# Optimization experiments

Measured on AMD Instinct MI355X. Metric: run time of the kernel, lower is better.

The kernel has to match this reference:

```python
import jax, jax.numpy as jnp
import numpy as np
import math

PERIODS = [4, 2, 1]          # period_num[-3:] sorted desc
SEQ, PRED, CH = 192, 96, 8
TOPM, DM = 20, 512
N_TRAIN, BSZ = 10000, 32


def decompose_mg(data):
    # data: [N, L, C] -> mg: [P, N, L, C], offset-removed (last step per period)
    N, L, C = data.shape
    mgs = []
    for g in PERIODS:
        cur = data.reshape(N, L // g, g, C).mean(axis=2)   # pooled
        cur = jnp.repeat(cur, g, axis=1)                   # repeat_interleave
        mgs.append(cur)
    mg = jnp.stack(mgs, axis=0)                            # [P, N, L, C]
    offset = mg[:, :, -1:, :]
    return mg - offset


def l2norm(x, eps=1e-12):
    n = jnp.sqrt(jnp.sum(x * x, axis=-1, keepdims=True))
    return x / jnp.maximum(n, eps)


def setup_inputs() -> dict:
    key = jax.random.key(0)
    ks = jax.random.split(key, 10)
    F = SEQ * CH
    return {
        "x": jax.random.normal(ks[0], (BSZ, SEQ, CH), dtype=jnp.float32),
        "index": jax.random.randint(ks[1], (BSZ,), 0, N_TRAIN),
        "train_data_all": jax.random.normal(ks[2], (N_TRAIN, SEQ, CH), dtype=jnp.float32),
        "y_data_all": jax.random.normal(ks[3], (N_TRAIN, PRED, CH), dtype=jnp.float32),
        "W_sim": jax.random.normal(ks[4], (F, F), dtype=jnp.float32) / math.sqrt(F),
        "b_sim": jax.random.normal(ks[5], (F,), dtype=jnp.float32) * 0.01,
        "Wq": jax.random.normal(ks[6], (CH, DM), dtype=jnp.float32) / math.sqrt(CH),
        "bq": jax.random.normal(ks[7], (DM,), dtype=jnp.float32) * 0.01,
        "Wk": jax.random.normal(ks[8], (CH, DM), dtype=jnp.float32) / math.sqrt(CH),
        "bk": jax.random.normal(ks[9], (DM,), dtype=jnp.float32) * 0.01,
    }


def reference(x, index, train_data_all, y_data_all, W_sim, b_sim, Wq, bq, Wk, bk):
    P = len(PERIODS)
    bsz = x.shape[0]
    n_train = train_data_all.shape[0]

    # multi-period decomposition (prepare_dataset + retrieve)
    train_mg = decompose_mg(train_data_all)   # [P, N, SEQ, CH]
    y_mg = decompose_mg(y_data_all)           # [P, N, PRED, CH]
    x_mg = decompose_mg(x)                    # [P, B, SEQ, CH]

    # periodic_batch_corr: shared linear then cosine similarity
    bx = x_mg.reshape(P, bsz, -1) @ W_sim + b_sim           # [P, B, F]
    ax = train_mg.reshape(P, n_train, -1) @ W_sim + b_sim   # [P, N, F]
    sim = jnp.einsum('pbf,pnf->pbn', l2norm(bx), l2norm(ax))

    # self-exclusion sliding mask (train=True)
    win = 2 * (SEQ + PRED) - 1
    slid = jnp.arange(win)[None, :] + (index - SEQ - PRED + 1)[:, None]
    slid = jnp.clip(slid, 0, n_train - 1)
    mask = jnp.zeros((bsz, n_train), dtype=bool).at[
        jnp.arange(bsz)[:, None], slid].set(True)
    sim = jnp.where(mask[None], -jnp.inf, sim)

    # top-m retrieval
    _, topm_idx = jax.lax.top_k(sim, TOPM)                  # [P, B, TOPM]

    # gather neighbors per period
    gather = jax.vmap(lambda src, i: src[i])                # over period axis
    k = gather(train_mg, topm_idx)                          # [P, B, M, SEQ, CH]
    v = gather(y_mg, topm_idx)                              # [P, B, M, PRED, CH]

    # cross attention (shared projections across periods)
    q_emb = x_mg @ Wq + bq                                  # [P, B, S, D]
    k_emb = k @ Wk + bk                                     # [P, B, M, T, D]
    scores = jnp.einsum('pbsd,pbmtd->pbsmt', q_emb, k_emb) / math.sqrt(DM)
    S = scores.shape[2]
    w = jax.nn.softmax(scores.reshape(P, bsz, S, TOPM * S), axis=-1)
    w = w.reshape(P, bsz, S, TOPM, S)
    nw = w.sum(axis=-1).sum(axis=2)                         # [P, B, M]
    nw = jax.nn.softmax(nw, axis=-1)
    out = jnp.einsum('pbm,pbmlc->pblc', nw, v)              # [P, B, PRED, CH]
    return out
```

## Files before the change

### kernel.cpp

```cpp
#include <hip/hip_runtime.h>
#include <hip/hip_bf16.h>
#include <math.h>

#define NPER 3
#define SEQL 192
#define PREDL 96
#define CH 8
#define FD 1536
#define NT 10000
#define BS 32
#define PB 96
#define TOPM 20
#define DM 512
#define HALFW 287
#define NROWS 30000
#define NRP2 10112
#define NRB2 79
#define NCB 12
#define PCOLS 24
#define NWG2 (NRB2*NCB)
#define NJ 3840
#define K0R 384
#define K1R 768
#define K2R 1536
#define KS 16
#define NCH 8
#define CHSZ (NT/NCH)
#define NWTG 4080
#define NB_DOT (3*NRB2)
#define BUFSZ (2*128*32)
#define RSQRT_DM 0.04419417382415922f

typedef __attribute__((ext_vector_type(8))) short bf16x8;
typedef __attribute__((ext_vector_type(4))) float f32x4;
typedef __attribute__((address_space(3))) short lds_short_t;
typedef __attribute__((address_space(1))) const short glb_short_t;

__device__ inline float bflo(unsigned u){ return __uint_as_float(u << 16); }
__device__ inline float bfhi(unsigned u){ return __uint_as_float(u & 0xFFFF0000u); }
__device__ inline float bf2f(unsigned short u){ return __uint_as_float((unsigned)u << 16); }
__device__ inline unsigned short f2bf(float v){
  __hip_bfloat16 h = __float2bfloat16(v);
  return *reinterpret_cast<unsigned short*>(&h);
}

template<int L>
__device__ __forceinline__ void dec_body(const float* __restrict__ data,
                                         float* __restrict__ mg,
                                         __hip_bfloat16* __restrict__ m0,
                                         __hip_bfloat16* __restrict__ m1,
                                         __hip_bfloat16* __restrict__ m2,
                                         __hip_bfloat16* __restrict__ trH,
                                         __hip_bfloat16* __restrict__ trL,
                                         int N, int n, float* fpool) {
  float* row = fpool;
  float* m4  = fpool + L*CH;
  float* m2s = fpool + L*CH + (L/4)*CH;
  const float* src = data + (size_t)n*L*CH;
  for (int e = threadIdx.x; e < L*CH/4; e += 256)
    *reinterpret_cast<float4*>(&row[e*4]) = *reinterpret_cast<const float4*>(&src[e*4]);
  __syncthreads();
  for (int i = threadIdx.x; i < (L/4)*CH; i += 256) {
    int j = i >> 3, c = i & 7;
    m4[i] = (row[(4*j)*CH+c] + row[(4*j+1)*CH+c] + row[(4*j+2)*CH+c] + row[(4*j+3)*CH+c]) * 0.25f;
  }
  for (int i = threadIdx.x; i < (L/2)*CH; i += 256) {
    int j = i >> 3, c = i & 7;
    m2s[i] = (row[(2*j)*CH+c] + row[(2*j+1)*CH+c]) * 0.5f;
  }
  __syncthreads();
  if (mg) {
    size_t plane = (size_t)N*L*CH;
    size_t base  = (size_t)n*L*CH;
    for (int e = threadIdx.x; e < L*CH/4; e += 256) {
      int i = e*4;
      int l = i >> 3, c0 = i & 7;
      float v0[4], v1[4], v2[4];
      #pragma unroll
      for (int j=0;j<4;j++) {
        int c = c0 + j;
        v0[j] = m4[(l>>2)*CH+c] - m4[(L/4-1)*CH+c];
        v1[j] = m2s[(l>>1)*CH+c] - m2s[(L/2-1)*CH+c];
        v2[j] = row[i+j] - row[(L-1)*CH+c];
      }
      *reinterpret_cast<float4*>(&mg[base+i])           = make_float4(v0[0],v0[1],v0[2],v0[3]);
      *reinterpret_cast<float4*>(&mg[plane+base+i])     = make_float4(v1[0],v1[1],v1[2],v1[3]);
      *reinterpret_cast<float4*>(&mg[2*plane+base+i])   = make_float4(v2[0],v2[1],v2[2],v2[3]);
    }
  }
  if (m0) {
    unsigned short* p0 = (unsigned short*)m0 + (size_t)n*K0R;
    unsigned short* p1 = (unsigned short*)m1 + (size_t)n*K1R;
    unsigned short* p2 = (unsigned short*)m2 + (size_t)n*K2R;
    for (int e = threadIdx.x; e < K0R/4; e += 256) {
      int i = e*4, c0 = i & 7;
      ushort4 u;
      u.x = f2bf(m4[i]   - m4[(L/4-1)*CH + c0]);
      u.y = f2bf(m4[i+1] - m4[(L/4-1)*CH + c0+1]);
      u.z = f2bf(m4[i+2] - m4[(L/4-1)*CH + c0+2]);
      u.w = f2bf(m4[i+3] - m4[(L/4-1)*CH + c0+3]);
      *reinterpret_cast<ushort4*>(&p0[i]) = u;
    }
    for (int e = threadIdx.x; e < K1R/4; e += 256) {
      int i = e*4, c0 = i & 7;
      ushort4 u;
      u.x = f2bf(m2s[i]   - m2s[(L/2-1)*CH + c0]);
      u.y = f2bf(m2s[i+1] - m2s[(L/2-1)*CH + c0+1]);
      u.z = f2bf(m2s[i+2] - m2s[(L/2-1)*CH + c0+2]);
      u.w = f2bf(m2s[i+3] - m2s[(L/2-1)*CH + c0+3]);
      *reinterpret_cast<ushort4*>(&p1[i]) = u;
    }
    for (int e = threadIdx.x; e < K2R/4; e += 256) {
      int i = e*4, c0 = i & 7;
      ushort4 u;
      u.x = f2bf(row[i]   - row[(L-1)*CH + c0]);
      u.y = f2bf(row[i+1] - row[(L-1)*CH + c0+1]);
      u.z = f2bf(row[i+2] - row[(L-1)*CH + c0+2]);
      u.w = f2bf(row[i+3] - row[(L-1)*CH + c0+3]);
      *reinterpret_cast<ushort4*>(&p2[i]) = u;
    }
  }
  if (trH) {
    unsigned short* h = (unsigned short*)trH + (size_t)n*L*CH;
    unsigned short* l = (unsigned short*)trL + (size_t)n*L*CH;
    for (int e = threadIdx.x; e < L*CH/4; e += 256) {
      int i = e*4;
      ushort4 uh, ul;
      uh.x = f2bf(row[i]);   ul.x = f2bf(row[i]   - bf2f(uh.x));
      uh.y = f2bf(row[i+1]); ul.y = f2bf(row[i+1] - bf2f(uh.y));
      uh.z = f2bf(row[i+2]); ul.z = f2bf(row[i+2] - bf2f(uh.z));
      uh.w = f2bf(row[i+3]); ul.w = f2bf(row[i+3] - bf2f(uh.w));
      *reinterpret_cast<ushort4*>(&h[i]) = uh;
      *reinterpret_cast<ushort4*>(&l[i]) = ul;
    }
  }
}

__device__ __forceinline__ void wtg_body(const float* __restrict__ W,
                                         __hip_bfloat16* __restrict__ wt0,
                                         __hip_bfloat16* __restrict__ wt1,
                                         __hip_bfloat16* __restrict__ wt2,
                                         const float* __restrict__ Wq,
                                         const float* __restrict__ bq,
                                         const float* __restrict__ Wk,
                                         const float* __restrict__ bk,
                                         float* __restrict__ cst,
                                         int wb, float* fpool) {
  int bxx = wb / 48, byy = wb % 48;
  if (bxx == 84) {
    if (byy != 0) return;
    int tt = threadIdx.x;
    if (tt < 64) {
      int c = tt >> 3, e = tt & 7;
      float s = 0.f;
      for (int d=0; d<DM; d++) s += Wq[c*DM+d] * Wk[e*DM+d];
      cst[tt] = s;
    } else if (tt < 72) {
      int c = tt - 64; float s=0.f;
      for (int d=0;d<DM;d++) s += Wq[c*DM+d]*bk[d];
      cst[tt] = s;
    } else if (tt < 80) {
      int e = tt - 72; float s=0.f;
      for (int d=0;d<DM;d++) s += Wk[e*DM+d]*bq[d];
      cst[tt] = s;
    } else if (tt == 80) {
      float s=0.f;
      for (int d=0;d<DM;d++) s += bq[d]*bk[d];
      cst[80] = s;
    }
    return;
  }
  int G, kr0, Kred;
  __hip_bfloat16* Wt;
  if (bxx < 12)      { G = 4; kr0 = bxx*32;      Kred = K0R; Wt = wt0; }
  else if (bxx < 36) { G = 2; kr0 = (bxx-12)*32; Kred = K1R; Wt = wt1; }
  else               { G = 1; kr0 = (bxx-36)*32; Kred = K2R; Wt = wt2; }
  int f0 = byy*32;
  int k0 = kr0*G;
  int tid = threadIdx.x, tx = tid & 31, ty = tid >> 5;
  for (int i = ty; i < 32*G; i += 8)
    fpool[i*33 + tx] = W[(size_t)(k0+i)*FD + f0 + tx];
  __syncthreads();
  for (int fl = ty; fl < 32; fl += 8) {
    float s = 0.f;
    for (int i=0;i<G;i++) s += fpool[(((tx>>3)*G+i)*8 + (tx&7))*33 + fl];
    Wt[(size_t)(f0+fl)*Kred + kr0 + tx] = __float2bfloat16(s);
  }
}

__global__ __launch_bounds__(256) void k_front(const float* __restrict__ x,
                                               const float* __restrict__ train,
                                               float* __restrict__ x_mg,
                                               __hip_bfloat16* __restrict__ m0,
                                               __hip_bfloat16* __restrict__ m1,
                                               __hip_bfloat16* __restrict__ m2,
                                               __hip_bfloat16* __restrict__ trH,
                                               __hip_bfloat16* __restrict__ trL,
                                               const float* __restrict__ W,
                                               __hip_bfloat16* __restrict__ wt0,
                                               __hip_bfloat16* __restrict__ wt1,
                                               __hip_bfloat16* __restrict__ wt2,
                                               const float* __restrict__ Wq,
                                               const float* __restrict__ bq,
                                               const float* __restrict__ Wk,
                                               const float* __restrict__ bk,
                                               float* __restrict__ cst) {
  __shared__ float fpool[128*33];
  int bid = blockIdx.x;
  if (bid < NT) {
    dec_body<SEQL>(train, nullptr, m0, m1, m2, trH, trL, NT, bid, fpool);
  } else if (bid < NT + NWTG) {
    wtg_body(W, wt0, wt1, wt2, Wq, bq, Wk, bk, cst, bid - NT, fpool);
  } else {
    dec_body<SEQL>(x, x_mg, nullptr, nullptr, nullptr, nullptr, nullptr,
                   BS, bid - NT - NWTG, fpool);
  }
}

__global__ __launch_bounds__(256) void k_bx_part(const float* __restrict__ xmg,
                                                 const float* __restrict__ W,
                                                 float* __restrict__ bxp) {
  __shared__ float xs[PB][17];
  __shared__ float Ws[16][65];
  int f0 = blockIdx.x * 64;
  int ks = blockIdx.y;
  int kbase = ks * (FD/KS);
  int tid = threadIdx.x;
  int fl = tid & 63, gp = tid >> 6;
  float acc[24];
  #pragma unroll
  for (int j=0;j<24;j++) acc[j]=0.f;
  for (int k0 = kbase; k0 < kbase + FD/KS; k0 += 16) {
    for (int e = tid; e < PB*16; e += 256) {
      int r = e >> 4, k = e & 15;
      xs[r][k] = xmg[(size_t)r*FD + k0 + k];
    }
    for (int e = tid; e < 16*64; e += 256) {
      int k = e >> 6, f = e & 63;
      Ws[k][f] = W[(size_t)(k0+k)*FD + f0 + f];
    }
    __syncthreads();
    #pragma unroll
    for (int kk = 0; kk < 16; kk++) {
      float w = Ws[kk][fl];
      #pragma unroll
      for (int j=0;j<24;j++) acc[j] += w * xs[gp + 4*j][kk];
    }
    __syncthreads();
  }
  #pragma unroll
  for (int j=0;j<24;j++) {
    int pb = gp + 4*j;
    bxp[((size_t)ks*PB + pb)*FD + f0 + fl] = acc[j];
  }
}

__global__ __launch_bounds__(256) void k_bxnorm(const float* __restrict__ bxp,
                                                const float* __restrict__ bsim,
                                                float* __restrict__ u_out,
                                                float* __restrict__ cpb) {
  __shared__ float rowv[FD];
  __shared__ float r1[256], r2[256];
  __shared__ float invs;
  int pb = blockIdx.x, tid = threadIdx.x;
  float s2 = 0.f, sb = 0.f;
  for (int f = tid; f < FD; f += 256) {
    float s = 0.f;
    #pragma unroll
    for (int ks=0; ks<KS; ks++) s += bxp[((size_t)ks*PB + pb)*FD + f];
    s += bsim[f];
    rowv[f] = s;
    s2 += s*s; sb += s*bsim[f];
  }
  r1[tid]=s2; r2[tid]=sb; __syncthreads();
  for (int off=128; off>0; off>>=1) {
    if (tid<off) { r1[tid]+=r1[tid+off]; r2[tid]+=r2[tid+off]; }
    __syncthreads();
  }
  if (tid==0) {
    float iv = 1.f / fmaxf(sqrtf(r1[0]), 1e-12f);
    invs = iv;
    cpb[pb] = r2[0] * iv;
  }
  __syncthreads();
  float iv = invs;
  for (int f = tid; f < FD; f += 256) u_out[(size_t)pb*FD + f] = rowv[f]*iv;
}

__global__ __launch_bounds__(256) void k_t_part(const float* __restrict__ u,
                                                const float* __restrict__ W,
                                                float* __restrict__ tp) {
  __shared__ float us[PB][17];
  __shared__ float Wt[64][17];
  int k0 = blockIdx.x * 64;
  int ks = blockIdx.y;
  int fbase = ks * (FD/KS);
  int tid = threadIdx.x;
  int kl = tid & 63, gp = tid >> 6;
  float acc[24];
  #pragma unroll
  for (int j=0;j<24;j++) acc[j]=0.f;
  for (int fc = fbase; fc < fbase + FD/KS; fc += 16) {
    for (int e = tid; e < PB*16; e += 256) {
      int r = e >> 4, f = e & 15;
      us[r][f] = u[(size_t)r*FD + fc + f];
    }
    for (int e = tid; e < 64*16; e += 256) {
      int k = e >> 4, f = e & 15;
      Wt[k][f] = W[(size_t)(k0+k)*FD + fc + f];
    }
    __syncthreads();
    #pragma unroll
    for (int ff = 0; ff < 16; ff++) {
      float w = Wt[kl][ff];
      #pragma unroll
      for (int j=0;j<24;j++) acc[j] += w * us[gp + 4*j][ff];
    }
    __syncthreads();
  }
  #pragma unroll
  for (int j=0;j<24;j++) {
    int pb = gp + 4*j;
    tp[((size_t)ks*PB + pb)*FD + k0 + kl] = acc[j];
  }
}

__global__ __launch_bounds__(192) void k_tred_adj(const float* __restrict__ tp,
                                                  __hip_bfloat16* __restrict__ tadjH,
                                                  __hip_bfloat16* __restrict__ tadjL) {
  __shared__ float ts[SEQL*CH];
  __shared__ float Tc[CH];
  int pb = blockIdx.x;
  int p = pb / BS;
  int g = (p==0) ? 4 : (p==1) ? 2 : 1;
  int l = threadIdx.x;
  #pragma unroll
  for (int c=0;c<CH;c++) {
    float s = 0.f;
    #pragma unroll
    for (int ks=0; ks<KS; ks++) s += tp[((size_t)ks*PB + pb)*FD + l*CH + c];
    ts[l*CH+c] = s;
  }
  __syncthreads();
  if (l < CH) {
    float s=0.f;
    for (int j=0;j<SEQL;j++) s += ts[j*CH+l];
    Tc[l] = s;
  }
  __syncthreads();
  int j0 = (l/g)*g;
  bool last = (j0 == SEQL-g);
  float ig = 1.f/(float)g;
  unsigned short* th = (unsigned short*)tadjH;
  unsigned short* tl = (unsigned short*)tadjL;
  #pragma unroll
  for (int c=0;c<CH;c++) {
    float s = 0.f;
    for (int jj=0;jj<g;jj++) s += ts[(j0+jj)*CH+c];
    float v = s*ig - (last ? Tc[c]*ig : 0.f);
    unsigned short hv = f2bf(v);
    th[(size_t)pb*FD + l*CH+c] = hv;
    tl[(size_t)pb*FD + l*CH+c] = f2bf(v - bf2f(hv));
  }
}

#define PIPE_SYNC_4()  do { asm volatile("s_waitcnt vmcnt(4)" ::: "memory"); \
                            __builtin_amdgcn_s_barrier(); \
                            __builtin_amdgcn_sched_barrier(0); } while(0)
#define PIPE_SYNC_0()  do { asm volatile("s_waitcnt vmcnt(0)" ::: "memory"); \
                            __builtin_amdgcn_s_barrier(); \
                            __builtin_amdgcn_sched_barrier(0); } while(0)

__device__ __forceinline__ void norm_body(const short* __restrict__ A,
                                          const short* __restrict__ B,
                                          int K, int p, int seg,
                                          const float* __restrict__ bsim,
                                          float* __restrict__ part,
                                          short* pool) {
  int q = NWG2 >> 3, r = NWG2 & 7;
  int xcd = seg & 7, pos = seg >> 3;
  int wgid = (xcd < r ? xcd*(q+1) : r*(q+1) + (xcd-r)*q) + pos;
  int rb = wgid / NCB, cb = wgid - rb*NCB;
  int row0 = rb*128, col0 = cb*128;
  int tid = threadIdx.x, lane = tid & 63, wid = tid >> 6;
  int wr = (wid>>1)*64, wc = (wid&1)*64;

  size_t aoff[2], boff[2];
  int ldsb[2];
  #pragma unroll
  for (int i=0;i<2;i++) {
    int lrow = (wid*2+i)*16 + (lane>>2);
    int sl = lane & 3;
    int ss = (sl - lrow - (lrow>>2)) & 3;
    aoff[i] = (size_t)(row0 + lrow)*K + 8*ss;
    boff[i] = (size_t)(col0 + lrow)*K + 8*ss;
    ldsb[i] = (wid*2+i)*16*32;
  }

  f32x4 acc[4][4];
  #pragma unroll
  for (int m=0;m<4;m++)
    #pragma unroll
    for (int n=0;n<4;n++) acc[m][n] = (f32x4){0.f,0.f,0.f,0.f};

  int kslot = lane >> 4;
  int nt = K >> 5;
  #pragma unroll
  for (int i=0;i<2;i++) {
    __builtin_amdgcn_global_load_lds((glb_short_t*)(A + aoff[i]),
                                     (lds_short_t*)&pool[ldsb[i]], 16, 0, 0);
    __builtin_amdgcn_global_load_lds((glb_short_t*)(B + boff[i]),
                                     (lds_short_t*)&pool[128*32 + ldsb[i]], 16, 0, 0);
  }
  #pragma unroll
  for (int i=0;i<2;i++) {
    __builtin_amdgcn_global_load_lds((glb_short_t*)(A + aoff[i] + 32),
                                     (lds_short_t*)&pool[BUFSZ + ldsb[i]], 16, 0, 0);
    __builtin_amdgcn_global_load_lds((glb_short_t*)(B + boff[i] + 32),
                                     (lds_short_t*)&pool[BUFSZ + 128*32 + ldsb[i]], 16, 0, 0);
  }
  PIPE_SYNC_4();
  int cur = 0;
  for (int t = 0; t < nt; ++t) {
    if (t + 2 < nt) {
      int nx = cur + 2; if (nx >= 3) nx -= 3;
      short* nb = pool + nx*BUFSZ;
      int kn = (t+2) << 5;
      #pragma unroll
      for (int i=0;i<2;i++) {
        __builtin_amdgcn_global_load_lds((glb_short_t*)(A + aoff[i] + kn),
                                         (lds_short_t*)&nb[ldsb[i]], 16, 0, 0);
        __builtin_amdgcn_global_load_lds((glb_short_t*)(B + boff[i] + kn),
                                         (lds_short_t*)&nb[128*32 + ldsb[i]], 16, 0, 0);
      }
    }
    const short* lA = pool + cur*BUFSZ;
    const short* lB = lA + 128*32;
    bf16x8 af[4], bfr[4];
    #pragma unroll
    for (int m=0;m<4;m++) {
      int rr = wr + m*16 + (lane&15);
      int s = (kslot + rr + (rr>>2)) & 3;
      af[m] = *(const bf16x8*)&lA[rr*32 + s*8];
    }
    #pragma unroll
    for (int n=0;n<4;n++) {
      int rr = wc + n*16 + (lane&15);
      int s = (kslot + rr + (rr>>2)) & 3;
      bfr[n] = *(const bf16x8*)&lB[rr*32 + s*8];
    }
    #pragma unroll
    for (int m=0;m<4;m++)
      #pragma unroll
      for (int n=0;n<4;n++)
        acc[m][n] = __builtin_amdgcn_mfma_f32_16x16x32_bf16(af[m], bfr[n], acc[m][n], 0, 0, 0);
    if (t + 1 < nt) {
      if (t + 2 < nt) PIPE_SYNC_4(); else PIPE_SYNC_0();
    }
    cur = (cur + 1 == 3) ? 0 : cur + 1;
  }

  float bv[4];
  #pragma unroll
  for (int n=0;n<4;n++) bv[n] = bsim[col0 + wc + n*16 + (lane&15)];
  int pslot = cb*2 + (wid&1);
  #pragma unroll
  for (int m=0;m<4;m++) {
    #pragma unroll
    for (int j=0;j<4;j++) {
      float s = 0.f;
      #pragma unroll
      for (int n=0;n<4;n++) { float v = acc[m][n][j] + bv[n]; s += v*v; }
      s += __shfl_xor(s, 1); s += __shfl_xor(s, 2);
      s += __shfl_xor(s, 4); s += __shfl_xor(s, 8);
      if ((lane & 15) == 0) {
        int rr = row0 + wr + m*16 + (lane>>4)*4 + j;
        part[((size_t)p*NRP2 + rr)*PCOLS + pslot] = s;
      }
    }
  }
}

__device__ __forceinline__ void dot_body(const short* __restrict__ A,
                                         const short* __restrict__ B,
                                         float* __restrict__ dst,
                                         int cbn, short* pool) {
  int col0 = cbn * 128;
  int tid = threadIdx.x, lane = tid & 63, wid = tid >> 6;
  int wr = (wid>>1)*64, wc = (wid&1)*64;

  size_t aoff[2], boff[2];
  int ldsb[2];
  #pragma unroll
  for (int i=0;i<2;i++) {
    int lrow = (wid*2+i)*16 + (lane>>2);
    int sl = lane & 3;
    int ss = (sl - lrow - (lrow>>2)) & 3;
    aoff[i] = (size_t)lrow*FD + 8*ss;
    boff[i] = (size_t)(col0 + lrow)*FD + 8*ss;
    ldsb[i] = (wid*2+i)*16*32;
  }

  f32x4 acc[4][4];
  #pragma unroll
  for (int m=0;m<4;m++)
    #pragma unroll
    for (int n=0;n<4;n++) acc[m][n] = (f32x4){0.f,0.f,0.f,0.f};

  int kslot = lane >> 4;
  const int nt = FD >> 5;
  #pragma unroll
  for (int i=0;i<2;i++) {
    __builtin_amdgcn_global_load_lds((glb_short_t*)(A + aoff[i]),
                                     (lds_short_t*)&pool[ldsb[i]], 16, 0, 0);
    __builtin_amdgcn_global_load_lds((glb_short_t*)(B + boff[i]),
                                     (lds_short_t*)&pool[128*32 + ldsb[i]], 16, 0, 0);
  }
  #pragma unroll
  for (int i=0;i<2;i++) {
    __builtin_amdgcn_global_load_lds((glb_short_t*)(A + aoff[i] + 32),
                                     (lds_short_t*)&pool[BUFSZ + ldsb[i]], 16, 0, 0);
    __builtin_amdgcn_global_load_lds((glb_short_t*)(B + boff[i] + 32),
                                     (lds_short_t*)&pool[BUFSZ + 128*32 + ldsb[i]], 16, 0, 0);
  }
  PIPE_SYNC_4();
  int cur = 0;
  for (int t = 0; t < nt; ++t) {
    if (t + 2 < nt) {
      int nx = cur + 2; if (nx >= 3) nx -= 3;
      short* nb = pool + nx*BUFSZ;
      int kn = (t+2) << 5;
      #pragma unroll
      for (int i=0;i<2;i++) {
        __builtin_amdgcn_global_load_lds((glb_short_t*)(A + aoff[i] + kn),
                                         (lds_short_t*)&nb[ldsb[i]], 16, 0, 0);
        __builtin_amdgcn_global_load_lds((glb_short_t*)(B + boff[i] + kn),
                                         (lds_short_t*)&nb[128*32 + ldsb[i]], 16, 0, 0);
      }
    }
    const short* lA = pool + cur*BUFSZ;
    const short* lB = lA + 128*32;
    bf16x8 af[4], bfr[4];
    #pragma unroll
    for (int m=0;m<4;m++) {
      int rr = wr + m*16 + (lane&15);
      int s = (kslot + rr + (rr>>2)) & 3;
      af[m] = *(const bf16x8*)&lA[rr*32 + s*8];
    }
    #pragma unroll
    for (int n=0;n<4;n++) {
      int rr = wc + n*16 + (lane&15);
      int s = (kslot + rr + (rr>>2)) & 3;
      bfr[n] = *(const bf16x8*)&lB[rr*32 + s*8];
    }
    #pragma unroll
    for (int m=0;m<4;m++)
      #pragma unroll
      for (int n=0;n<4;n++)
        acc[m][n] = __builtin_amdgcn_mfma_f32_16x16x32_bf16(af[m], bfr[n], acc[m][n], 0, 0, 0);
    if (t + 1 < nt) {
      if (t + 2 < nt) PIPE_SYNC_4(); else PIPE_SYNC_0();
    }
    cur = (cur + 1 == 3) ? 0 : cur + 1;
  }

  #pragma unroll
  for (int m=0;m<4;m++) {
    int prow = wr + m*16 + (lane>>4)*4;
    if (prow >= PB) continue;
    #pragma unroll
    for (int n=0;n<4;n++) {
      int ncol = col0 + wc + n*16 + (lane&15);
      if (ncol >= NT) continue;
      #pragma unroll
      for (int j=0;j<4;j++) {
        dst[(size_t)(prow + j)*NT + ncol] = acc[m][n][j];
      }
    }
  }
}

__global__ __launch_bounds__(256) void k_gemms(
    const __hip_bfloat16* __restrict__ A0b, const __hip_bfloat16* __restrict__ A1b,
    const __hip_bfloat16* __restrict__ A2b,
    const __hip_bfloat16* __restrict__ B0b, const __hip_bfloat16* __restrict__ B1b,
    const __hip_bfloat16* __restrict__ B2b,
    const float* __restrict__ bsim, float* __restrict__ part,
    const __hip_bfloat16* __restrict__ tadjHb, const __hip_bfloat16* __restrict__ tadjLb,
    const __hip_bfloat16* __restrict__ trHb, const __hip_bfloat16* __restrict__ trLb,
    float* __restrict__ dotp3) {
  __shared__ __align__(16) short pool[3*BUFSZ];
  int bid = blockIdx.x;
  if (bid < NB_DOT) {
    int term = bid / NRB2, cbn = bid - term*NRB2;
    const short* A = (term == 2) ? (const short*)tadjLb : (const short*)tadjHb;
    const short* B = (term == 1) ? (const short*)trLb   : (const short*)trHb;
    dot_body(A, B, dotp3 + (size_t)term*PB*NT, cbn, pool);
  } else if (bid < NB_DOT + NWG2) {
    norm_body((const short*)A2b, (const short*)B2b, K2R, 2, bid - NB_DOT, bsim, part, pool);
  } else if (bid < NB_DOT + 2*NWG2) {
    norm_body((const short*)A1b, (const short*)B1b, K1R, 1, bid - NB_DOT - NWG2, bsim, part, pool);
  } else {
    norm_body((const short*)A0b, (const short*)B0b, K0R, 0,
              bid - NB_DOT - 2*NWG2, bsim, part, pool);
  }
}

__global__ __launch_bounds__(256) void k_norm_red(const float* __restrict__ part,
                                                  float* __restrict__ norm2) {
  int r = blockIdx.x*256 + threadIdx.x;
  if (r < NROWS) {
    int p = r / NT, rr = r - p*NT;
    float s=0.f;
    #pragma unroll
    for (int cb=0; cb<PCOLS; cb++) s += part[((size_t)p*NRP2 + rr)*PCOLS + cb];
    norm2[r] = s;
  }
}

__global__ __launch_bounds__(256) void k_topk_part(const float* __restrict__ dotp3,
                                                   const float* __restrict__ cpb,
                                                   const float* __restrict__ norm2,
                                                   const int* __restrict__ index,
                                                   float* __restrict__ cv,
                                                   int* __restrict__ ci) {
  __shared__ float vals[CHSZ];
  __shared__ float rv[4];
  __shared__ int   ri[4];
  int pb = blockIdx.x, ch = blockIdx.y;
  int p = pb / BS, b = pb - p*BS;
  int n0 = ch*CHSZ;
  int tid = threadIdx.x, lane = tid & 63, wv = tid >> 6;
  int idx = index[b];
  int bl = idx - HALFW; if (bl < 0) bl = 0;
  int bh = idx + HALFW; if (bh > NT-1) bh = NT-1;
  const float* n2 = norm2 + (size_t)p*NT;
  float cp = cpb[pb];
  for (int i = tid; i < CHSZ; i += 256) {
    int n = n0 + i;
    float d = dotp3[(size_t)pb*NT + n]
            + dotp3[(size_t)PB*NT + (size_t)pb*NT + n]
            + dotp3[2*(size_t)PB*NT + (size_t)pb*NT + n] + cp;
    float v = d / fmaxf(sqrtf(n2[n]), 1e-12f);
    if (n >= bl && n <= bh) v = -INFINITY;
    vals[i] = v;
  }
  __syncthreads();
  for (int it = 0; it < TOPM; it++) {
    float bv = -INFINITY; int bi = CHSZ;
    for (int i = tid; i < CHSZ; i += 256) {
      float v = vals[i];
      if (v > bv) { bv = v; bi = i; }
    }
    #pragma unroll
    for (int off=32; off>0; off>>=1) {
      float ov = __shfl_xor(bv, off);
      int   oi = __shfl_xor(bi, off);
      if (ov > bv || (ov == bv && oi < bi)) { bv = ov; bi = oi; }
    }
    if (lane == 0) { rv[wv] = bv; ri[wv] = bi; }
    __syncthreads();
    if (tid == 0) {
      float fv = rv[0]; int fi = ri[0];
      #pragma unroll
      for (int w2=1; w2<4; w2++)
        if (rv[w2] > fv || (rv[w2] == fv && ri[w2] < fi)) { fv = rv[w2]; fi = ri[w2]; }
      cv[(pb*NCH + ch)*TOPM + it] = fv;
      ci[(pb*NCH + ch)*TOPM + it] = n0 + fi;
      vals[fi] = -INFINITY;
    }
    __syncthreads();
  }
}

__global__ __launch_bounds__(64) void k_topk_merge(const float* __restrict__ cv,
                                                   const int* __restrict__ ci,
                                                   int* __restrict__ topm) {
  __shared__ float v[NCH*TOPM];
  __shared__ int   id[NCH*TOPM];
  int pb = blockIdx.x;
  int lane = threadIdx.x;
  for (int i = lane; i < NCH*TOPM; i += 64) {
    v[i]  = cv[pb*NCH*TOPM + i];
    id[i] = ci[pb*NCH*TOPM + i];
  }
  __syncthreads();
  for (int it = 0; it < TOPM; it++) {
    float bv = -INFINITY; int bi = 0x7fffffff;
    for (int i = lane; i < NCH*TOPM; i += 64) {
      float vv = v[i];
      int ii = id[i];
      if (vv > bv || (vv == bv && ii < bi)) { bv = vv; bi = ii; }
    }
    #pragma unroll
    for (int off=32; off>0; off>>=1) {
      float ov = __shfl_xor(bv, off);
      int   oi = __shfl_xor(bi, off);
      if (ov > bv || (ov == bv && oi < bi)) { bv = ov; bi = oi; }
    }
    if (lane == 0) topm[pb*TOPM + it] = bi;
    for (int i = lane; i < NCH*TOPM; i += 64)
      if (id[i] == bi) v[i] = -INFINITY;
    __syncthreads();
  }
}

__device__ __forceinline__ void v_body(const float* __restrict__ ydata,
                                       const int* __restrict__ topm,
                                       float* __restrict__ vbuf,
                                       int bm, float* bpool) {
  float* row = bpool;
  float* m4  = bpool + 768;
  float* m2  = bpool + 960;
  int pb = bm / TOPM;
  int p = pb / BS;
  int n = topm[bm];
  int tid = threadIdx.x;
  const float* src = ydata + (size_t)n*PREDL*CH;
  for (int i=tid; i<PREDL*CH; i+=256) row[i]=src[i];
  __syncthreads();
  for (int i=tid; i<(PREDL/4)*CH; i+=256) {
    int j=i>>3, c=i&7;
    m4[i] = (row[(4*j)*CH+c]+row[(4*j+1)*CH+c]+row[(4*j+2)*CH+c]+row[(4*j+3)*CH+c])*0.25f;
  }
  for (int i=tid; i<(PREDL/2)*CH; i+=256) {
    int j=i>>3, c=i&7;
    m2[i] = (row[(2*j)*CH+c]+row[(2*j+1)*CH+c])*0.5f;
  }
  __syncthreads();
  float* dst = vbuf + (size_t)bm*PREDL*CH;
  for (int i=tid; i<PREDL*CH; i+=256) {
    int l=i>>3, c=i&7;
    float v;
    if (p==0)      v = m4[(l>>2)*CH+c] - m4[(PREDL/4-1)*CH+c];
    else if (p==1) v = m2[(l>>1)*CH+c] - m2[(PREDL/2-1)*CH+c];
    else           v = row[i] - row[(PREDL-1)*CH+c];
    dst[i] = v;
  }
}

template<int SH>
__device__ __forceinline__ void scores_body(
    const short* __restrict__ plane, int Kp,
    int pb, int sg,
    const int* __restrict__ topm,
    const float* __restrict__ xmg,
    const float* __restrict__ cst,
    float* __restrict__ nws,
    float* sc, int* tl, float* wred, float* lcst) {
  constexpr int UNQ = SEQL >> SH;
  constexpr int J   = TOPM * UNQ;
  constexpr int NU  = (J + 255) >> 8;
  constexpr bool FULL = (J % 256 == 0);
  int tid = threadIdx.x;
  int lane = tid & 63, wv = tid >> 6;
  if (tid < TOPM) tl[tid] = topm[pb*TOPM + tid];
  if (tid >= 32 && tid < 32+81) lcst[tid-32] = cst[tid-32];
  __syncthreads();
  uint4 kreg[NU];
  #pragma unroll
  for (int u=0; u<NU; u++) {
    int j = tid + u*256;
    if (FULL || j < J) {
      int m = j / UNQ, jj = j - m*UNQ;
      kreg[u] = *reinterpret_cast<const uint4*>(plane + (size_t)tl[m]*Kp + jj*8);
    }
  }
  for (int s8 = 0; s8 < 8; s8++) {
    int s = sg*8 + s8;
    int qr = pb*SEQL + s;
    float4 qa = *reinterpret_cast<const float4*>(&xmg[(size_t)qr*8]);
    float4 qc = *reinterpret_cast<const float4*>(&xmg[(size_t)qr*8+4]);
    float xq[8] = {qa.x,qa.y,qa.z,qa.w,qc.x,qc.y,qc.z,qc.w};
    float q[8];
    #pragma unroll
    for (int e=0;e<8;e++) {
      float ss = lcst[72+e];
      #pragma unroll
      for (int c=0;c<8;c++) ss += xq[c]*lcst[c*8+e];
      q[e] = ss;
    }
    float qb_s = lcst[80];
    #pragma unroll
    for (int c=0;c<8;c++) qb_s += xq[c]*lcst[64+c];
    float ms[NU];
    float lmax = -INFINITY;
    #pragma unroll
    for (int u=0; u<NU; u++) {
      int j = tid + u*256;
      if (FULL || j < J) {
        uint4 w = kreg[u];
        float s0 = qb_s;
        s0 += q[0]*bflo(w.x) + q[1]*bfhi(w.x);
        s0 += q[2]*bflo(w.y) + q[3]*bfhi(w.y);
        s0 += q[4]*bflo(w.z) + q[5]*bfhi(w.z);
        s0 += q[6]*bflo(w.w) + q[7]*bfhi(w.w);
        s0 *= RSQRT_DM;
        ms[u] = s0;
        lmax = fmaxf(lmax, s0);
      } else ms[u] = -INFINITY;
    }
    #pragma unroll
    for (int off=32; off>0; off>>=1) lmax = fmaxf(lmax, __shfl_xor(lmax, off));
    if (lane==0) wred[wv] = lmax;
    __syncthreads();
    float mx = fmaxf(fmaxf(wred[0],wred[1]),fmaxf(wred[2],wred[3]));
    float lsum = 0.f;
    #pragma unroll
    for (int u=0; u<NU; u++) {
      int j = tid + u*256;
      if (FULL || j < J) {
        float e = __expf(ms[u]-mx);
        sc[j] = e;
        lsum += e;
      }
    }
    #pragma unroll
    for (int off=32; off>0; off>>=1) lsum += __shfl_xor(lsum, off);
    if (lane==0) wred[4+wv] = lsum;
    __syncthreads();
    float invZ = 1.f / (wred[4]+wred[5]+wred[6]+wred[7]);
    for (int m = wv; m < TOPM; m += 4) {
      float v = 0.f;
      #pragma unroll
      for (int jj = 0; jj < UNQ; jj += 64) {
        int j2 = jj + lane;
        if (UNQ % 64 == 0 || j2 < UNQ) v += sc[m*UNQ + j2];
      }
      #pragma unroll
      for (int off=32; off>0; off>>=1) v += __shfl_xor(v, off);
      if (lane==0) nws[((size_t)pb*SEQL + s)*TOPM + m] = v * invZ;
    }
    __syncthreads();
  }
}

__global__ __launch_bounds__(256) void k_back(const __hip_bfloat16* __restrict__ m0,
                                              const __hip_bfloat16* __restrict__ m1,
                                              const __hip_bfloat16* __restrict__ m2,
                                              const int* __restrict__ topm,
                                              const float* __restrict__ xmg,
                                              const float* __restrict__ cst,
                                              float* __restrict__ nws,
                                              const float* __restrict__ ydata,
                                              float* __restrict__ vbuf) {
  __shared__ float bpool[3968];
  int bid = blockIdx.x;
  if (bid < PB*24) {
    int pb = bid / 24, sg = bid - (bid/24)*24;
    int p = pb / BS;
    float* sc = bpool;
    int* tl = (int*)(bpool + 3840);
    float* wred = bpool + 3864;
    float* lcst = bpool + 3872;
    if (p == 0)
      scores_body<2>((const short*)m0, K0R, pb, sg, topm, xmg, cst, nws, sc, tl, wred, lcst);
    else if (p == 1)
      scores_body<1>((const short*)m1, K1R, pb, sg, topm, xmg, cst, nws, sc, tl, wred, lcst);
    else
      scores_body<0>((const short*)m2, K2R, pb, sg, topm, xmg, cst, nws, sc, tl, wred, lcst);
  } else {
    v_body(ydata, topm, vbuf, bid - PB*24, bpool);
  }
}

__global__ __launch_bounds__(256) void k_out(const float* __restrict__ nws,
                                             const float* __restrict__ vbuf,
                                             float* __restrict__ out) {
  __shared__ float nwp[TOPM];
  __shared__ float nwf[TOPM];
  int pb = blockIdx.x;
  int tid = threadIdx.x;
  if (tid < TOPM) {
    float s=0.f;
    for (int ss=0; ss<SEQL; ss++) s += nws[((size_t)pb*SEQL+ss)*TOPM + tid];
    nwp[tid] = s;
  }
  __syncthreads();
  if (tid==0) {
    float mx=-INFINITY;
    for (int m=0;m<TOPM;m++) mx=fmaxf(mx,nwp[m]);
    float Z=0.f;
    for (int m=0;m<TOPM;m++){ float e=expf(nwp[m]-mx); nwf[m]=e; Z+=e; }
    float iz=1.f/Z;
    for (int m=0;m<TOPM;m++) nwf[m]*=iz;
  }
  __syncthreads();
  for (int i=tid; i<PREDL*CH; i+=256) {
    float o=0.f;
    #pragma unroll
    for (int m=0;m<TOPM;m++) o += nwf[m]*vbuf[((size_t)pb*TOPM+m)*PREDL*CH + i];
    out[(size_t)pb*PREDL*CH + i] = o;
  }
}

extern "C" void kernel_launch(void* const* d_in, const int* in_sizes, int n_in,
                              void* d_out, int out_size, void* d_ws, size_t ws_size,
                              hipStream_t stream) {
  const float* x     = (const float*)d_in[0];
  const int*   index = (const int*)  d_in[1];
  const float* train = (const float*)d_in[2];
  const float* ydata = (const float*)d_in[3];
  const float* Wsim  = (const float*)d_in[4];
  const float* bsim  = (const float*)d_in[5];
  const float* Wq    = (const float*)d_in[6];
  const float* bq    = (const float*)d_in[7];
  const float* Wk    = (const float*)d_in[8];
  const float* bk    = (const float*)d_in[9];
  float* out = (float*)d_out;

  float* ws = (float*)d_ws;
  size_t off = 0;
  auto alloc = [&](size_t n)->float* { float* pp = ws + off; off += (n + 63) & ~(size_t)63; return pp; };
  __hip_bfloat16* m0b = (__hip_bfloat16*)alloc((size_t)NRP2*K0R/2);
  __hip_bfloat16* m1b = (__hip_bfloat16*)alloc((size_t)NRP2*K1R/2);
  __hip_bfloat16* m2b = (__hip_bfloat16*)alloc((size_t)NRP2*K2R/2);
  __hip_bfloat16* wt0 = (__hip_bfloat16*)alloc((size_t)FD*K0R/2);
  __hip_bfloat16* wt1 = (__hip_bfloat16*)alloc((size_t)FD*K1R/2);
  __hip_bfloat16* wt2 = (__hip_bfloat16*)alloc((size_t)FD*K2R/2);
  __hip_bfloat16* trH = (__hip_bfloat16*)alloc((size_t)NRP2*FD/2);
  __hip_bfloat16* trL = (__hip_bfloat16*)alloc((size_t)NRP2*FD/2);
  __hip_bfloat16* tadjH = (__hip_bfloat16*)alloc((size_t)128*FD/2);
  __hip_bfloat16* tadjL = (__hip_bfloat16*)alloc((size_t)128*FD/2);
  float* x_mg     = alloc((size_t)NPER*BS*FD);
  float* bx       = alloc((size_t)PB*FD);
  float* cpb      = alloc(PB);
  float* gpart    = alloc((size_t)KS*PB*FD);
  float* part     = alloc((size_t)NPER*NRP2*PCOLS);
  float* norm2    = alloc(NROWS);
  float* dotp3    = alloc((size_t)3*PB*NT);
  float* cv       = alloc((size_t)PB*NCH*TOPM);
  int*   ci       = (int*)alloc(PB*NCH*TOPM);
  int*   topm     = (int*)alloc(PB*TOPM);
  float* cst      = alloc(128);
  float* vbuf     = alloc((size_t)PB*TOPM*PREDL*CH);
  float* nws      = alloc((size_t)PB*SEQL*TOPM);
  if (off * sizeof(float) > ws_size) return;

  k_front<<<NT + NWTG + BS, 256, 0, stream>>>(x, train, x_mg, m0b, m1b, m2b, trH, trL,
                                              Wsim, wt0, wt1, wt2, Wq, bq, Wk, bk, cst);
  k_bx_part<<<dim3(24, KS), 256, 0, stream>>>(x_mg, Wsim, gpart);
  k_bxnorm<<<PB, 256, 0, stream>>>(gpart, bsim, bx, cpb);
  k_t_part<<<dim3(24, KS), 256, 0, stream>>>(bx, Wsim, gpart);
  k_tred_adj<<<PB, 192, 0, stream>>>(gpart, tadjH, tadjL);
  k_gemms<<<NB_DOT + 3*NWG2, 256, 0, stream>>>(m0b, m1b, m2b, wt0, wt1, wt2, bsim, part,
                                               tadjH, tadjL, trH, trL, dotp3);
  k_norm_red<<<(NROWS+255)/256, 256, 0, stream>>>(part, norm2);
  k_topk_part<<<dim3(PB, NCH), 256, 0, stream>>>(dotp3, cpb, norm2, index, cv, ci);
  k_topk_merge<<<PB, 64, 0, stream>>>(cv, ci, topm);
  k_back<<<PB*24 + PB*TOPM, 256, 0, stream>>>(m0b, m1b, m2b, topm, x_mg, cst, nws,
                                              ydata, vbuf);
  k_out<<<PB, 256, 0, stream>>>(nws, vbuf, out);
}
```

Measured before the change: 405.0 us.

## Use 256x256 tiles with 512 threads for norm GEMMs, reorder block schedule

Each norm GEMM workgroup now covers a 256x256 output tile with 8 waves instead of 128x128 with 4 waves. Row padding grows to 10240 and the partial-norm slots are remapped to match. The dot GEMM keeps its 128x128 tile but is split across 8 waves with smaller per-wave fragments. The launch order is changed so the heaviest K=1536 and K=768 norm blocks start first, with the dot and K=384 blocks after. The larger tile is meant to raise operand reuse and cut global/LDS traffic per FLOP. In exchange the triple-buffered LDS pool grows to about 96 KB per block, which lowers occupancy and adds register pressure from the 8x4 accumulators.

```diff
diff --git a/kernel.cpp b/kernel.cpp
--- a/kernel.cpp
+++ b/kernel.cpp
@@ -14,12 +14,12 @@
 #define DM 512
 #define HALFW 287
 #define NROWS 30000
-#define NRP2 10112
+#define NRP3 10240
+#define NRB3 40
+#define NCB3 6
+#define PCOLS 24
+#define NWG3 (NRB3*NCB3)
 #define NRB2 79
-#define NCB 12
-#define PCOLS 24
-#define NWG2 (NRB2*NCB)
-#define NJ 3840
 #define K0R 384
 #define K1R 768
 #define K2R 1536
@@ -28,7 +28,8 @@
 #define CHSZ (NT/NCH)
 #define NWTG 4080
 #define NB_DOT (3*NRB2)
-#define BUFSZ (2*128*32)
+#define BUFSZ3 (2*256*32)
+#define BUFSZD (2*128*32)
 #define RSQRT_DM 0.04419417382415922f
 
 typedef __attribute__((ext_vector_type(8))) short bf16x8;
@@ -367,6 +368,9 @@
 #define PIPE_SYNC_4()  do { asm volatile("s_waitcnt vmcnt(4)" ::: "memory"); \
                             __builtin_amdgcn_s_barrier(); \
                             __builtin_amdgcn_sched_barrier(0); } while(0)
+#define PIPE_SYNC_2()  do { asm volatile("s_waitcnt vmcnt(2)" ::: "memory"); \
+                            __builtin_amdgcn_s_barrier(); \
+                            __builtin_amdgcn_sched_barrier(0); } while(0)
 #define PIPE_SYNC_0()  do { asm volatile("s_waitcnt vmcnt(0)" ::: "memory"); \
                             __builtin_amdgcn_s_barrier(); \
                             __builtin_amdgcn_sched_barrier(0); } while(0)
@@ -377,29 +381,30 @@
                                           const float* __restrict__ bsim,
                                           float* __restrict__ part,
                                           short* pool) {
-  int q = NWG2 >> 3, r = NWG2 & 7;
+  int q = NWG3 >> 3, r = NWG3 & 7;
   int xcd = seg & 7, pos = seg >> 3;
   int wgid = (xcd < r ? xcd*(q+1) : r*(q+1) + (xcd-r)*q) + pos;
-  int rb = wgid / NCB, cb = wgid - rb*NCB;
-  int row0 = rb*128, col0 = cb*128;
+  int rb = wgid / NCB3, cb = wgid - rb*NCB3;
+  int row0 = rb*256, col0 = cb*256;
   int tid = threadIdx.x, lane = tid & 63, wid = tid >> 6;
-  int wr = (wid>>1)*64, wc = (wid&1)*64;
+  int wm = wid >> 2, wn = wid & 3;
 
   size_t aoff[2], boff[2];
-  int ldsb[2];
+  int ldsA[2], ldsB[2];
   #pragma unroll
   for (int i=0;i<2;i++) {
-    int lrow = (wid*2+i)*16 + (lane>>2);
+    int lrow = (i*8 + wid)*16 + (lane>>2);
     int sl = lane & 3;
     int ss = (sl - lrow - (lrow>>2)) & 3;
     aoff[i] = (size_t)(row0 + lrow)*K + 8*ss;
     boff[i] = (size_t)(col0 + lrow)*K + 8*ss;
-    ldsb[i] = (wid*2+i)*16*32;
-  }
-
-  f32x4 acc[4][4];
-  #pragma unroll
-  for (int m=0;m<4;m++)
+    ldsA[i] = (i*8 + wid)*16*32;
+    ldsB[i] = 256*32 + (i*8 + wid)*16*32;
+  }
+
+  f32x4 acc[8][4];
+  #pragma unroll
+  for (int m=0;m<8;m++)
     #pragma unroll
     for (int n=0;n<4;n++) acc[m][n] = (f32x4){0.f,0.f,0.f,0.f};
 
@@ -408,49 +413,49 @@
   #pragma unroll
   for (int i=0;i<2;i++) {
     __builtin_amdgcn_global_load_lds((glb_short_t*)(A + aoff[i]),
-                                     (lds_short_t*)&pool[ldsb[i]], 16, 0, 0);
+                                     (lds_short_t*)&pool[ldsA[i]], 16, 0, 0);
     __builtin_amdgcn_global_load_lds((glb_short_t*)(B + boff[i]),
-                                     (lds_short_t*)&pool[128*32 + ldsb[i]], 16, 0, 0);
+                                     (lds_short_t*)&pool[ldsB[i]], 16, 0, 0);
   }
   #pragma unroll
   for (int i=0;i<2;i++) {
     __builtin_amdgcn_global_load_lds((glb_short_t*)(A + aoff[i] + 32),
-                                     (lds_short_t*)&pool[BUFSZ + ldsb[i]], 16, 0, 0);
+                                     (lds_short_t*)&pool[BUFSZ3 + ldsA[i]], 16, 0, 0);
     __builtin_amdgcn_global_load_lds((glb_short_t*)(B + boff[i] + 32),
-                                     (lds_short_t*)&pool[BUFSZ + 128*32 + ldsb[i]], 16, 0, 0);
+                                     (lds_short_t*)&pool[BUFSZ3 + ldsB[i]], 16, 0, 0);
   }
   PIPE_SYNC_4();
   int cur = 0;
   for (int t = 0; t < nt; ++t) {
     if (t + 2 < nt) {
       int nx = cur + 2; if (nx >= 3) nx -= 3;
-      short* nb = pool + nx*BUFSZ;
+      short* nb = pool + nx*BUFSZ3;
       int kn = (t+2) << 5;
       #pragma unroll
       for (int i=0;i<2;i++) {
         __builtin_amdgcn_global_load_lds((glb_short_t*)(A + aoff[i] + kn),
-                                         (lds_short_t*)&nb[ldsb[i]], 16, 0, 0);
+                                         (lds_short_t*)&nb[ldsA[i]], 16, 0, 0);
         __builtin_amdgcn_global_load_lds((glb_short_t*)(B + boff[i] + kn),
-                                         (lds_short_t*)&nb[128*32 + ldsb[i]], 16, 0, 0);
+                                         (lds_short_t*)&nb[ldsB[i]], 16, 0, 0);
       }
     }
-    const short* lA = pool + cur*BUFSZ;
-    const short* lB = lA + 128*32;
-    bf16x8 af[4], bfr[4];
-    #pragma unroll
-    for (int m=0;m<4;m++) {
-      int rr = wr + m*16 + (lane&15);
+    const short* lA = pool + cur*BUFSZ3;
+    const short* lB = lA + 256*32;
+    bf16x8 af[8], bfr[4];
+    #pragma unroll
+    for (int m=0;m<8;m++) {
+      int rr = wm*128 + m*16 + (lane&15);
       int s = (kslot + rr + (rr>>2)) & 3;
       af[m] = *(const bf16x8*)&lA[rr*32 + s*8];
     }
     #pragma unroll
     for (int n=0;n<4;n++) {
-      int rr = wc + n*16 + (lane&15);
+      int rr = wn*64 + n*16 + (lane&15);
       int s = (kslot + rr + (rr>>2)) & 3;
       bfr[n] = *(const bf16x8*)&lB[rr*32 + s*8];
     }
     #pragma unroll
-    for (int m=0;m<4;m++)
+    for (int m=0;m<8;m++)
       #pragma unroll
       for (int n=0;n<4;n++)
         acc[m][n] = __builtin_amdgcn_mfma_f32_16x16x32_bf16(af[m], bfr[n], acc[m][n], 0, 0, 0);
@@ -462,10 +467,10 @@
 
   float bv[4];
   #pragma unroll
-  for (int n=0;n<4;n++) bv[n] = bsim[col0 + wc + n*16 + (lane&15)];
-  int pslot = cb*2 + (wid&1);
-  #pragma unroll
-  for (int m=0;m<4;m++) {
+  for (int n=0;n<4;n++) bv[n] = bsim[col0 + wn*64 + n*16 + (lane&15)];
+  int pslot = cb*4 + wn;
+  #pragma unroll
+  for (int m=0;m<8;m++) {
     #pragma unroll
     for (int j=0;j<4;j++) {
       float s = 0.f;
@@ -474,8 +479,8 @@
       s += __shfl_xor(s, 1); s += __shfl_xor(s, 2);
       s += __shfl_xor(s, 4); s += __shfl_xor(s, 8);
       if ((lane & 15) == 0) {
-        int rr = row0 + wr + m*16 + (lane>>4)*4 + j;
-        part[((size_t)p*NRP2 + rr)*PCOLS + pslot] = s;
+        int rr = row0 + wm*128 + m*16 + (lane>>4)*4 + j;
+        part[((size_t)p*NRP3 + rr)*PCOLS + pslot] = s;
       }
     }
   }
@@ -487,90 +492,77 @@
                                          int cbn, short* pool) {
   int col0 = cbn * 128;
   int tid = threadIdx.x, lane = tid & 63, wid = tid >> 6;
-  int wr = (wid>>1)*64, wc = (wid&1)*64;
-
-  size_t aoff[2], boff[2];
-  int ldsb[2];
-  #pragma unroll
-  for (int i=0;i<2;i++) {
-    int lrow = (wid*2+i)*16 + (lane>>2);
-    int sl = lane & 3;
-    int ss = (sl - lrow - (lrow>>2)) & 3;
-    aoff[i] = (size_t)lrow*FD + 8*ss;
-    boff[i] = (size_t)(col0 + lrow)*FD + 8*ss;
-    ldsb[i] = (wid*2+i)*16*32;
-  }
-
-  f32x4 acc[4][4];
+  int wm = wid >> 2, wn = wid & 3;
+
+  int lrow = wid*16 + (lane>>2);
+  int sl = lane & 3;
+  int ss = (sl - lrow - (lrow>>2)) & 3;
+  size_t aoff = (size_t)lrow*FD + 8*ss;
+  size_t boff = (size_t)(col0 + lrow)*FD + 8*ss;
+  int ldsA = wid*16*32;
+  int ldsB = 128*32 + wid*16*32;
+
+  f32x4 acc[4][2];
   #pragma unroll
   for (int m=0;m<4;m++)
     #pragma unroll
-    for (int n=0;n<4;n++) acc[m][n] = (f32x4){0.f,0.f,0.f,0.f};
+    for (int n=0;n<2;n++) acc[m][n] = (f32x4){0.f,0.f,0.f,0.f};
 
   int kslot = lane >> 4;
   const int nt = FD >> 5;
-  #pragma unroll
-  for (int i=0;i<2;i++) {
-    __builtin_amdgcn_global_load_lds((glb_short_t*)(A + aoff[i]),
-                                     (lds_short_t*)&pool[ldsb[i]], 16, 0, 0);
-    __builtin_amdgcn_global_load_lds((glb_short_t*)(B + boff[i]),
-                                     (lds_short_t*)&pool[128*32 + ldsb[i]], 16, 0, 0);
-  }
-  #pragma unroll
-  for (int i=0;i<2;i++) {
-    __builtin_amdgcn_global_load_lds((glb_short_t*)(A + aoff[i] + 32),
-                                     (lds_short_t*)&pool[BUFSZ + ldsb[i]], 16, 0, 0);
-    __builtin_amdgcn_global_load_lds((glb_short_t*)(B + boff[i] + 32),
-                                     (lds_short_t*)&pool[BUFSZ + 128*32 + ldsb[i]], 16, 0, 0);
-  }
-  PIPE_SYNC_4();
+  __builtin_amdgcn_global_load_lds((glb_short_t*)(A + aoff),
+                                   (lds_short_t*)&pool[ldsA], 16, 0, 0);
+  __builtin_amdgcn_global_load_lds((glb_short_t*)(B + boff),
+                                   (lds_short_t*)&pool[ldsB], 16, 0, 0);
+  __builtin_amdgcn_global_load_lds((glb_short_t*)(A + aoff + 32),
+                                   (lds_short_t*)&pool[BUFSZD + ldsA], 16, 0, 0);
+  __builtin_amdgcn_global_load_lds((glb_short_t*)(B + boff + 32),
+                                   (lds_short_t*)&pool[BUFSZD + ldsB], 16, 0, 0);
+  PIPE_SYNC_2();
   int cur = 0;
   for (int t = 0; t < nt; ++t) {
     if (t + 2 < nt) {
       int nx = cur + 2; if (nx >= 3) nx -= 3;
-      short* nb = pool + nx*BUFSZ;
+      short* nb = pool + nx*BUFSZD;
       int kn = (t+2) << 5;
-      #pragma unroll
-      for (int i=0;i<2;i++) {
-        __builtin_amdgcn_global_load_lds((glb_short_t*)(A + aoff[i] + kn),
-                                         (lds_short_t*)&nb[ldsb[i]], 16, 0, 0);
-        __builtin_amdgcn_global_load_lds((glb_short_t*)(B + boff[i] + kn),
-                                         (lds_short_t*)&nb[128*32 + ldsb[i]], 16, 0, 0);
-      }
-    }
-    const short* lA = pool + cur*BUFSZ;
+      __builtin_amdgcn_global_load_lds((glb_short_t*)(A + aoff + kn),
+                                       (lds_short_t*)&nb[ldsA], 16, 0, 0);
+      __builtin_amdgcn_global_load_lds((glb_short_t*)(B + boff + kn),
+                                       (lds_short_t*)&nb[ldsB], 16, 0, 0);
+    }
+    const short* lA = pool + cur*BUFSZD;
     const short* lB = lA + 128*32;
-    bf16x8 af[4], bfr[4];
+    bf16x8 af[4], bfr[2];
     #pragma unroll
     for (int m=0;m<4;m++) {
-      int rr = wr + m*16 + (lane&15);
+      int rr = wm*64 + m*16 + (lane&15);
       int s = (kslot + rr + (rr>>2)) & 3;
       af[m] = *(const bf16x8*)&lA[rr*32 + s*8];
     }
     #pragma unroll
-    for (int n=0;n<4;n++) {
-      int rr = wc + n*16 + (lane&15);
+    for (int n=0;n<2;n++) {
+      int rr = wn*32 + n*16 + (lane&15);
       int s = (kslot + rr + (rr>>2)) & 3;
       bfr[n] = *(const bf16x8*)&lB[rr*32 + s*8];
     }
     #pragma unroll
     for (int m=0;m<4;m++)
       #pragma unroll
-      for (int n=0;n<4;n++)
+      for (int n=0;n<2;n++)
         acc[m][n] = __builtin_amdgcn_mfma_f32_16x16x32_bf16(af[m], bfr[n], acc[m][n], 0, 0, 0);
     if (t + 1 < nt) {
-      if (t + 2 < nt) PIPE_SYNC_4(); else PIPE_SYNC_0();
+      if (t + 2 < nt) PIPE_SYNC_2(); else PIPE_SYNC_0();
     }
     cur = (cur + 1 == 3) ? 0 : cur + 1;
   }
 
   #pragma unroll
   for (int m=0;m<4;m++) {
-    int prow = wr + m*16 + (lane>>4)*4;
+    int prow = wm*64 + m*16 + (lane>>4)*4;
     if (prow >= PB) continue;
     #pragma unroll
-    for (int n=0;n<4;n++) {
-      int ncol = col0 + wc + n*16 + (lane&15);
+    for (int n=0;n<2;n++) {
+      int ncol = col0 + wn*32 + n*16 + (lane&15);
       if (ncol >= NT) continue;
       #pragma unroll
       for (int j=0;j<4;j++) {
@@ -580,7 +572,7 @@
   }
 }
 
-__global__ __launch_bounds__(256) void k_gemms(
+__global__ __launch_bounds__(512, 2) void k_gemms(
     const __hip_bfloat16* __restrict__ A0b, const __hip_bfloat16* __restrict__ A1b,
     const __hip_bfloat16* __restrict__ A2b,
     const __hip_bfloat16* __restrict__ B0b, const __hip_bfloat16* __restrict__ B1b,
@@ -589,20 +581,21 @@
     const __hip_bfloat16* __restrict__ tadjHb, const __hip_bfloat16* __restrict__ tadjLb,
     const __hip_bfloat16* __restrict__ trHb, const __hip_bfloat16* __restrict__ trLb,
     float* __restrict__ dotp3) {
-  __shared__ __align__(16) short pool[3*BUFSZ];
+  __shared__ __align__(16) short pool[3*BUFSZ3];
   int bid = blockIdx.x;
-  if (bid < NB_DOT) {
-    int term = bid / NRB2, cbn = bid - term*NRB2;
+  if (bid < NWG3) {
+    norm_body((const short*)A2b, (const short*)B2b, K2R, 2, bid, bsim, part, pool);
+  } else if (bid < 2*NWG3) {
+    norm_body((const short*)A1b, (const short*)B1b, K1R, 1, bid - NWG3, bsim, part, pool);
+  } else if (bid < 2*NWG3 + NB_DOT) {
+    int d = bid - 2*NWG3;
+    int term = d / NRB2, cbn = d - term*NRB2;
     const short* A = (term == 2) ? (const short*)tadjLb : (const short*)tadjHb;
     const short* B = (term == 1) ? (const short*)trLb   : (const short*)trHb;
     dot_body(A, B, dotp3 + (size_t)term*PB*NT, cbn, pool);
-  } else if (bid < NB_DOT + NWG2) {
-    norm_body((const short*)A2b, (const short*)B2b, K2R, 2, bid - NB_DOT, bsim, part, pool);
-  } else if (bid < NB_DOT + 2*NWG2) {
-    norm_body((const short*)A1b, (const short*)B1b, K1R, 1, bid - NB_DOT - NWG2, bsim, part, pool);
   } else {
     norm_body((const short*)A0b, (const short*)B0b, K0R, 0,
-              bid - NB_DOT - 2*NWG2, bsim, part, pool);
+              bid - 2*NWG3 - NB_DOT, bsim, part, pool);
   }
 }
 
@@ -613,7 +606,7 @@
     int p = r / NT, rr = r - p*NT;
     float s=0.f;
     #pragma unroll
-    for (int cb=0; cb<PCOLS; cb++) s += part[((size_t)p*NRP2 + rr)*PCOLS + cb];
+    for (int cb=0; cb<PCOLS; cb++) s += part[((size_t)p*NRP3 + rr)*PCOLS + cb];
     norm2[r] = s;
   }
 }
@@ -912,21 +905,21 @@
   float* ws = (float*)d_ws;
   size_t off = 0;
   auto alloc = [&](size_t n)->float* { float* pp = ws + off; off += (n + 63) & ~(size_t)63; return pp; };
-  __hip_bfloat16* m0b = (__hip_bfloat16*)alloc((size_t)NRP2*K0R/2);
-  __hip_bfloat16* m1b = (__hip_bfloat16*)alloc((size_t)NRP2*K1R/2);
-  __hip_bfloat16* m2b = (__hip_bfloat16*)alloc((size_t)NRP2*K2R/2);
+  __hip_bfloat16* m0b = (__hip_bfloat16*)alloc((size_t)NRP3*K0R/2);
+  __hip_bfloat16* m1b = (__hip_bfloat16*)alloc((size_t)NRP3*K1R/2);
+  __hip_bfloat16* m2b = (__hip_bfloat16*)alloc((size_t)NRP3*K2R/2);
   __hip_bfloat16* wt0 = (__hip_bfloat16*)alloc((size_t)FD*K0R/2);
   __hip_bfloat16* wt1 = (__hip_bfloat16*)alloc((size_t)FD*K1R/2);
   __hip_bfloat16* wt2 = (__hip_bfloat16*)alloc((size_t)FD*K2R/2);
-  __hip_bfloat16* trH = (__hip_bfloat16*)alloc((size_t)NRP2*FD/2);
-  __hip_bfloat16* trL = (__hip_bfloat16*)alloc((size_t)NRP2*FD/2);
+  __hip_bfloat16* trH = (__hip_bfloat16*)alloc((size_t)(NRB2*128)*FD/2);
+  __hip_bfloat16* trL = (__hip_bfloat16*)alloc((size_t)(NRB2*128)*FD/2);
   __hip_bfloat16* tadjH = (__hip_bfloat16*)alloc((size_t)128*FD/2);
   __hip_bfloat16* tadjL = (__hip_bfloat16*)alloc((size_t)128*FD/2);
   float* x_mg     = alloc((size_t)NPER*BS*FD);
   float* bx       = alloc((size_t)PB*FD);
   float* cpb      = alloc(PB);
   float* gpart    = alloc((size_t)KS*PB*FD);
-  float* part     = alloc((size_t)NPER*NRP2*PCOLS);
+  float* part     = alloc((size_t)NPER*NRP3*PCOLS);
   float* norm2    = alloc(NROWS);
   float* dotp3    = alloc((size_t)3*PB*NT);
   float* cv       = alloc((size_t)PB*NCH*TOPM);
@@ -943,7 +936,7 @@
   k_bxnorm<<<PB, 256, 0, stream>>>(gpart, bsim, bx, cpb);
   k_t_part<<<dim3(24, KS), 256, 0, stream>>>(bx, Wsim, gpart);
   k_tred_adj<<<PB, 192, 0, stream>>>(gpart, tadjH, tadjL);
-  k_gemms<<<NB_DOT + 3*NWG2, 256, 0, stream>>>(m0b, m1b, m2b, wt0, wt1, wt2, bsim, part,
+  k_gemms<<<3*NWG3 + NB_DOT, 512, 0, stream>>>(m0b, m1b, m2b, wt0, wt1, wt2, bsim, part,
                                                tadjH, tadjL, trH, trL, dotp3);
   k_norm_red<<<(NROWS+255)/256, 256, 0, stream>>>(part, norm2);
   k_topk_part<<<dim3(PB, NCH), 256, 0, stream>>>(dotp3, cpb, norm2, index, cv, ci);
```

Measured after the change: 385.0 us. -4.9%, faster.
